# Kernel tuning notes

Hardware: AMD Instinct MI355X
Metric: run time of the kernel (lower is better)

## Reference

```python
import jax, jax.numpy as jnp
import numpy as np

MARGIN = 1.5  # init kwarg
N, M, K = 8192, 128, 16


def setup_inputs() -> dict:
    key = jax.random.key(0)
    k1, k2 = jax.random.split(key)
    feature = jax.random.normal(k1, (N, M), dtype=jnp.float32)
    # binary multi-labels in {0,1}; k=16 channels makes an all-zero row vanishingly rare
    label = jax.random.randint(k2, (N, K), 0, 2, dtype=jnp.int32)
    return {"feature": feature, "label": label}


def reference(feature, label):
    n, m = feature.shape
    # --- pair weights: IoU of positive label sets ------------------------
    # original: ((l_i == l_j) & (l_i > 0.5)).sum() / ((l_i > 0.5) | (l_j > 0.5)).sum()
    # for binary labels this is |pos_i & pos_j| / |pos_i | pos_j|
    pos = (label > 0).astype(jnp.float32)          # [n,k]
    npos = pos.sum(axis=1)                          # [n]
    inter = pos @ pos.T                             # [n,n] intersection counts
    union = npos[:, None] + npos[None, :] - inter   # [n,n] union counts
    weight = inter / union                          # 0/0 -> nan, same as torch
    weight = jnp.where(weight == 0, -1.0, weight)   # weight[weight==0] = -1
    # --- pairwise Euclidean distance via Gram trick ----------------------
    sq = jnp.sum(feature * feature, axis=1)         # [n]
    d2 = sq[:, None] + sq[None, :] - 2.0 * (feature @ feature.T)
    d2 = jnp.maximum(d2, 0.0)
    pos_d2 = d2 > 0
    dist = jnp.where(pos_d2, jnp.sqrt(jnp.where(pos_d2, d2, 1.0)), 0.0)
    dist = dist / np.sqrt(m).astype(np.float32)
    # --- margin-clipped weighted loss ------------------------------------
    loss = weight * jnp.minimum(dist, MARGIN)
    return loss.mean()
```

## Files before the change

### kernel.cpp

```cpp
#include <hip/hip_runtime.h>

#define NROW 8192
#define MDIM 128
#define KLAB 16
#define NSLAB 64
#define NSUPER (NSLAB*(NSLAB+1)/2)
#define NBLK (NSUPER*2)
#define MARGINP  16.970562748477139f
#define MARGINP2 288.0f

typedef __attribute__((ext_vector_type(8))) short  s16x8;
typedef __attribute__((ext_vector_type(4))) float  f32x4;

#if __has_builtin(__builtin_amdgcn_sqrtf)
#define FSQRT(x) __builtin_amdgcn_sqrtf(x)
#else
#define FSQRT(x) sqrtf(x)
#endif
#if __has_builtin(__builtin_amdgcn_rcpf)
#define FRCP(x) __builtin_amdgcn_rcpf(x)
#else
#define FRCP(x) (1.0f / (x))
#endif
#if __has_builtin(__builtin_amdgcn_fmed3f)
#define FCLAMP(x) __builtin_amdgcn_fmed3f((x), 0.0f, MARGINP2)
#else
#define FCLAMP(x) fminf(fmaxf((x), 0.0f), MARGINP2)
#endif

__device__ __forceinline__ unsigned short f2bf(float x) {
  unsigned u = __float_as_uint(x);
  return (unsigned short)((u + 0x7FFFu + ((u >> 16) & 1u)) >> 16);
}

__global__ void prep_kernel(const float* __restrict__ feat, const int* __restrict__ label,
                            unsigned short* __restrict__ fbf, float* __restrict__ sq,
                            int* __restrict__ maskA) {
  int wv = threadIdx.x >> 6, lane = threadIdx.x & 63;
  int sub = lane >> 4, l16 = lane & 15;
  int row = blockIdx.x * 16 + wv * 4 + sub;
  const float* rp = feat + (size_t)row * MDIM + l16 * 8;
  float4 va = *reinterpret_cast<const float4*>(rp);
  float4 vb = *reinterpret_cast<const float4*>(rp + 4);
  s16x8 st;
  st[0]=(short)f2bf(va.x); st[1]=(short)f2bf(va.y); st[2]=(short)f2bf(va.z); st[3]=(short)f2bf(va.w);
  st[4]=(short)f2bf(vb.x); st[5]=(short)f2bf(vb.y); st[6]=(short)f2bf(vb.z); st[7]=(short)f2bf(vb.w);
  *reinterpret_cast<s16x8*>(fbf + (size_t)row * MDIM + l16 * 8) = st;
  float s = va.x*va.x + va.y*va.y + va.z*va.z + va.w*va.w
          + vb.x*vb.x + vb.y*vb.y + vb.z*vb.z + vb.w*vb.w;
  #pragma unroll
  for (int off = 8; off >= 1; off >>= 1) s += __shfl_xor(s, off);
  int lab = label[((size_t)blockIdx.x * 16 + wv * 4) * KLAB + lane];
  unsigned long long bal = __ballot(lab > 0);
  if (l16 == 0) {
    sq[row]    = s;
    maskA[row] = (int)(unsigned)((bal >> (sub * 16)) & 0xFFFFull);
  }
}

__global__ __launch_bounds__(256, 4) void pair_main(
    const unsigned short* __restrict__ fbf, const float* __restrict__ sq,
    const int* __restrict__ maskA, float* __restrict__ part) {
  __shared__ char smem[32768];
  __shared__ float bsum[4];

  int orig = blockIdx.x;
  int swz = (orig & 7) * (NBLK / 8) + (orig >> 3);
  int sid = swz >> 1, half = swz & 1;

  int bi = 0, rem = sid;
  while (rem >= NSLAB - bi) { rem -= NSLAB - bi; bi++; }
  int bj = bi + rem;
  bool diag = (bi == bj);

  int wv = threadIdx.x >> 6, lane = threadIdx.x & 63;
  int l15 = lane & 15, lg = lane >> 4;
  int wr = wv >> 1, wc = wv & 1;

  const char* fb = (const char*)fbf;
  int arow = bi * 128 + half * 64 + wr * 32;

  s16x8 af[2][4];
  #pragma unroll
  for (int fi = 0; fi < 2; fi++)
    #pragma unroll
    for (int ks = 0; ks < 4; ks++)
      af[fi][ks] = *reinterpret_cast<const s16x8*>(
          fb + (size_t)(arow + fi * 16 + l15) * 256 + ks * 64 + lg * 16);

  float sqi[2][4]; int mi[2][4];
  #pragma unroll
  for (int fi = 0; fi < 2; fi++)
    #pragma unroll
    for (int r = 0; r < 4; r++) {
      int ir = arow + fi * 16 + lg * 4 + r;
      sqi[fi][r] = sq[ir]; mi[fi][r] = maskA[ir];
    }
  float sqj[4]; int mj[4];
  #pragma unroll
  for (int fj = 0; fj < 4; fj++) {
    int jr = bj * 128 + wc * 64 + fj * 16 + l15;
    sqj[fj] = sq[jr]; mj[fj] = maskA[jr];
  }

  {
    const char* gB = fb + (size_t)bj * 128 * 256;
    #pragma unroll
    for (int k = 0; k < 8; k++) {
      int f = threadIdx.x + 256 * k;
      int row = f >> 4, c = f & 15;
      s16x8 v = *reinterpret_cast<const s16x8*>(gB + row * 256 + c * 16);
      int wck = c ^ (row & 7);
      *reinterpret_cast<s16x8*>(smem + row * 256 + wck * 16) = v;
    }
  }
  __syncthreads();

  float sum = 0.0f;

  #pragma unroll
  for (int fj = 0; fj < 4; fj++) {
    s16x8 B[4];
    #pragma unroll
    for (int ks = 0; ks < 4; ks++) {
      int lr = wc * 64 + fj * 16 + l15;
      int rc = (ks * 4 + lg) ^ (lr & 7);
      B[ks] = *reinterpret_cast<const s16x8*>(smem + lr * 256 + rc * 16);
    }

    f32x4 acc[2];
    acc[0] = (f32x4){0.f,0.f,0.f,0.f}; acc[1] = (f32x4){0.f,0.f,0.f,0.f};
    #pragma unroll
    for (int ks = 0; ks < 4; ks++)
      #pragma unroll
      for (int fi = 0; fi < 2; fi++)
        acc[fi] = __builtin_amdgcn_mfma_f32_16x16x32_bf16(af[fi][ks], B[ks], acc[fi], 0, 0, 0);

    #pragma unroll
    for (int fi = 0; fi < 2; fi++)
      #pragma unroll
      for (int r = 0; r < 4; r++) {
        float g  = acc[fi][r];
        float d2 = fmaf(-2.0f, g, sqi[fi][r] + sqj[fj]);
        float t  = FSQRT(FCLAMP(d2));
        int inter = __popc(mi[fi][r] & mj[fj]);
        int uni   = __popc(mi[fi][r] | mj[fj]);
        float w = (float)inter * FRCP((float)uni);
        w = (inter == 0) ? -1.0f : w;
        if (diag) {
          int il = half * 64 + wr * 32 + fi * 16 + lg * 4 + r;
          int jl = wc * 64 + fj * 16 + l15;
          w *= (jl > il) ? 2.0f : ((jl == il) ? 1.0f : 0.0f);
        }
        sum = fmaf(w, t, sum);
      }
  }

  #pragma unroll
  for (int off = 32; off >= 1; off >>= 1) sum += __shfl_xor(sum, off);
  if (lane == 0) bsum[wv] = sum;
  __syncthreads();
  if (threadIdx.x == 0) {
    float s = bsum[0] + bsum[1] + bsum[2] + bsum[3];
    part[orig] = diag ? s : 2.0f * s;
  }
}

__global__ void reduce_kernel(const float* __restrict__ part, float* __restrict__ out) {
  int tid = threadIdx.x;
  double s = 0.0;
  for (int i = tid; i < NBLK; i += 256) s += (double)part[i];
  #pragma unroll
  for (int off = 32; off >= 1; off >>= 1) s += __shfl_xor(s, off);
  __shared__ double wsum[4];
  int wv = tid >> 6, lane = tid & 63;
  if (lane == 0) wsum[wv] = s;
  __syncthreads();
  if (tid == 0) {
    double t = wsum[0] + wsum[1] + wsum[2] + wsum[3];
    out[0] = (float)(t * (1.0 / (11.313708498984760 * 67108864.0)));
  }
}

extern "C" void kernel_launch(void* const* d_in, const int* in_sizes, int n_in,
                              void* d_out, int out_size, void* d_ws, size_t ws_size,
                              hipStream_t stream) {
  const float* feat  = (const float*)d_in[0];
  const int*   label = (const int*)d_in[1];
  char* ws = (char*)d_ws;
  float* part           = (float*)ws;
  float* sq             = (float*)(ws + 16896);
  int*   maskA          = (int*)(ws + 16896 + 32768);
  unsigned short* fbf   = (unsigned short*)(ws + 16896 + 65536);
  float* out = (float*)d_out;

  prep_kernel<<<NROW / 16, 256, 0, stream>>>(feat, label, fbf, sq, maskA);
  pair_main<<<NBLK, 256, 0, stream>>>(fbf, sq, maskA, part);
  reduce_kernel<<<1, 256, 0, stream>>>(part, out);
}
```

Before: 44.71 us.

## Shrink pair tiles to 64x64 triangular blocks and drop block swizzle

```diff
diff --git a/kernel.cpp b/kernel.cpp
--- a/kernel.cpp
+++ b/kernel.cpp
@@ -3,9 +3,8 @@
 #define NROW 8192
 #define MDIM 128
 #define KLAB 16
-#define NSLAB 64
-#define NSUPER (NSLAB*(NSLAB+1)/2)
-#define NBLK (NSUPER*2)
+#define NSLAB2 128
+#define NBLK2 (NSLAB2*(NSLAB2+1)/2)
 #define MARGINP  16.970562748477139f
 #define MARGINP2 288.0f
 
@@ -58,55 +57,45 @@
   }
 }
 
-__global__ __launch_bounds__(256, 4) void pair_main(
+__global__ __launch_bounds__(256, 6) void pair_main(
     const unsigned short* __restrict__ fbf, const float* __restrict__ sq,
     const int* __restrict__ maskA, float* __restrict__ part) {
-  __shared__ char smem[32768];
+  __shared__ char smem[16384];
   __shared__ float bsum[4];
 
-  int orig = blockIdx.x;
-  int swz = (orig & 7) * (NBLK / 8) + (orig >> 3);
-  int sid = swz >> 1, half = swz & 1;
-
-  int bi = 0, rem = sid;
-  while (rem >= NSLAB - bi) { rem -= NSLAB - bi; bi++; }
+  int bi = 0, rem = blockIdx.x;
+  while (rem >= NSLAB2 - bi) { rem -= NSLAB2 - bi; bi++; }
   int bj = bi + rem;
   bool diag = (bi == bj);
 
   int wv = threadIdx.x >> 6, lane = threadIdx.x & 63;
   int l15 = lane & 15, lg = lane >> 4;
-  int wr = wv >> 1, wc = wv & 1;
+  const char* fb = (const char*)fbf;
 
-  const char* fb = (const char*)fbf;
-  int arow = bi * 128 + half * 64 + wr * 32;
+  int arow = bi * 64 + wv * 16;
+  s16x8 af[4];
+  #pragma unroll
+  for (int ks = 0; ks < 4; ks++)
+    af[ks] = *reinterpret_cast<const s16x8*>(
+        fb + (size_t)(arow + l15) * 256 + ks * 64 + lg * 16);
 
-  s16x8 af[2][4];
+  float sqi[4]; int mi[4];
   #pragma unroll
-  for (int fi = 0; fi < 2; fi++)
-    #pragma unroll
-    for (int ks = 0; ks < 4; ks++)
-      af[fi][ks] = *reinterpret_cast<const s16x8*>(
-          fb + (size_t)(arow + fi * 16 + l15) * 256 + ks * 64 + lg * 16);
-
-  float sqi[2][4]; int mi[2][4];
-  #pragma unroll
-  for (int fi = 0; fi < 2; fi++)
-    #pragma unroll
-    for (int r = 0; r < 4; r++) {
-      int ir = arow + fi * 16 + lg * 4 + r;
-      sqi[fi][r] = sq[ir]; mi[fi][r] = maskA[ir];
-    }
+  for (int r = 0; r < 4; r++) {
+    int ir = arow + lg * 4 + r;
+    sqi[r] = sq[ir]; mi[r] = maskA[ir];
+  }
   float sqj[4]; int mj[4];
   #pragma unroll
   for (int fj = 0; fj < 4; fj++) {
-    int jr = bj * 128 + wc * 64 + fj * 16 + l15;
+    int jr = bj * 64 + fj * 16 + l15;
     sqj[fj] = sq[jr]; mj[fj] = maskA[jr];
   }
 
   {
-    const char* gB = fb + (size_t)bj * 128 * 256;
+    const char* gB = fb + (size_t)bj * 64 * 256;
     #pragma unroll
-    for (int k = 0; k < 8; k++) {
+    for (int k = 0; k < 4; k++) {
       int f = threadIdx.x + 256 * k;
       int row = f >> 4, c = f & 15;
       s16x8 v = *reinterpret_cast<const s16x8*>(gB + row * 256 + c * 16);
@@ -123,37 +112,32 @@
     s16x8 B[4];
     #pragma unroll
     for (int ks = 0; ks < 4; ks++) {
-      int lr = wc * 64 + fj * 16 + l15;
+      int lr = fj * 16 + l15;
       int rc = (ks * 4 + lg) ^ (lr & 7);
       B[ks] = *reinterpret_cast<const s16x8*>(smem + lr * 256 + rc * 16);
     }
 
-    f32x4 acc[2];
-    acc[0] = (f32x4){0.f,0.f,0.f,0.f}; acc[1] = (f32x4){0.f,0.f,0.f,0.f};
+    f32x4 acc = (f32x4){0.f,0.f,0.f,0.f};
     #pragma unroll
     for (int ks = 0; ks < 4; ks++)
-      #pragma unroll
-      for (int fi = 0; fi < 2; fi++)
-        acc[fi] = __builtin_amdgcn_mfma_f32_16x16x32_bf16(af[fi][ks], B[ks], acc[fi], 0, 0, 0);
+      acc = __builtin_amdgcn_mfma_f32_16x16x32_bf16(af[ks], B[ks], acc, 0, 0, 0);
 
     #pragma unroll
-    for (int fi = 0; fi < 2; fi++)
-      #pragma unroll
-      for (int r = 0; r < 4; r++) {
-        float g  = acc[fi][r];
-        float d2 = fmaf(-2.0f, g, sqi[fi][r] + sqj[fj]);
-        float t  = FSQRT(FCLAMP(d2));
-        int inter = __popc(mi[fi][r] & mj[fj]);
-        int uni   = __popc(mi[fi][r] | mj[fj]);
-        float w = (float)inter * FRCP((float)uni);
-        w = (inter == 0) ? -1.0f : w;
-        if (diag) {
-          int il = half * 64 + wr * 32 + fi * 16 + lg * 4 + r;
-          int jl = wc * 64 + fj * 16 + l15;
-          w *= (jl > il) ? 2.0f : ((jl == il) ? 1.0f : 0.0f);
-        }
-        sum = fmaf(w, t, sum);
+    for (int r = 0; r < 4; r++) {
+      float g  = acc[r];
+      float d2 = fmaf(-2.0f, g, sqi[r] + sqj[fj]);
+      float t  = FSQRT(FCLAMP(d2));
+      int inter = __popc(mi[r] & mj[fj]);
+      int uni   = __popc(mi[r] | mj[fj]);
+      float w = (float)inter * FRCP((float)uni);
+      w = (inter == 0) ? -1.0f : w;
+      if (diag) {
+        int il = wv * 16 + lg * 4 + r;
+        int jl = fj * 16 + l15;
+        w *= (jl > il) ? 2.0f : ((jl == il) ? 1.0f : 0.0f);
       }
+      sum = fmaf(w, t, sum);
+    }
   }
 
   #pragma unroll
@@ -162,14 +146,14 @@
   __syncthreads();
   if (threadIdx.x == 0) {
     float s = bsum[0] + bsum[1] + bsum[2] + bsum[3];
-    part[orig] = diag ? s : 2.0f * s;
+    part[blockIdx.x] = diag ? s : 2.0f * s;
   }
 }
 
 __global__ void reduce_kernel(const float* __restrict__ part, float* __restrict__ out) {
   int tid = threadIdx.x;
   double s = 0.0;
-  for (int i = tid; i < NBLK; i += 256) s += (double)part[i];
+  for (int i = tid; i < NBLK2; i += 256) s += (double)part[i];
   #pragma unroll
   for (int off = 32; off >= 1; off >>= 1) s += __shfl_xor(s, off);
   __shared__ double wsum[4];
@@ -189,12 +173,12 @@
   const int*   label = (const int*)d_in[1];
   char* ws = (char*)d_ws;
   float* part           = (float*)ws;
-  float* sq             = (float*)(ws + 16896);
-  int*   maskA          = (int*)(ws + 16896 + 32768);
-  unsigned short* fbf   = (unsigned short*)(ws + 16896 + 65536);
+  float* sq             = (float*)(ws + 33280);
+  int*   maskA          = (int*)(ws + 33280 + 32768);
+  unsigned short* fbf   = (unsigned short*)(ws + 33280 + 65536);
   float* out = (float*)d_out;
 
   prep_kernel<<<NROW / 16, 256, 0, stream>>>(feat, label, fbf, sq, maskA);
-  pair_main<<<NBLK, 256, 0, stream>>>(fbf, sq, maskA, part);
+  pair_main<<<NBLK2, 256, 0, stream>>>(fbf, sq, maskA, part);
   reduce_kernel<<<1, 256, 0, stream>>>(part, out);
 }
```

New measurement: 48.08 us. 7.5% more time.
